# Optimization experiments

Measured on AMD Instinct MI355X. Metric: run time of the kernel, lower is better.

## Reference

```python
import jax, jax.numpy as jnp
import numpy as np

K = 6
N_LEVELS = [200000, 50000, 12500]
CHANNELS = [3, 64, 128, 256]
DEGREE = 32
FANIN = 4          # each pooled node averages FANIN fine nodes (D values = 1/FANIN)
NUM_CLASSES = 10


def setup_inputs() -> dict:
    key = jax.random.key(0)
    ks = jax.random.split(key, 16)
    inp = {}
    inp["x"] = jax.random.normal(ks[0], (N_LEVELS[0], 3), dtype=jnp.float32)
    # random sparse connectivity per level (edge lists, COO)
    for i, n in enumerate(N_LEVELS):
        inp[f"edge_index{i}"] = jax.random.randint(ks[1 + i], (2, n * DEGREE), 0, n)
    # sparse downscale matrices: row r of D_i averages FANIN source nodes
    inp["pool_cols0"] = jax.random.randint(ks[4], (N_LEVELS[1] * FANIN,), 0, N_LEVELS[0])
    inp["pool_cols1"] = jax.random.randint(ks[5], (N_LEVELS[2] * FANIN,), 0, N_LEVELS[1])
    # ChebConv parameters: weight [K, in, out] (Glorot-ish), bias [out]
    for i in range(3):
        cin, cout = CHANNELS[i], CHANNELS[i + 1]
        scale = (2.0 / (cin + cout)) ** 0.5
        inp[f"w{i}"] = scale * jax.random.normal(ks[6 + 2 * i], (K, cin, cout), dtype=jnp.float32)
        inp[f"b{i}"] = jnp.zeros((cout,), dtype=jnp.float32)
    lin_in = N_LEVELS[-1] * CHANNELS[-1]
    inp["lw"] = jax.random.normal(ks[12], (NUM_CLASSES, lin_in), dtype=jnp.float32) * (1.0 / np.sqrt(lin_in))
    inp["lb"] = jnp.zeros((NUM_CLASSES,), dtype=jnp.float32)
    return inp


def cheb_conv(x, edge_index, weight, bias):
    """PyG ChebConv, sym normalization, lambda_max=2, unit edge weights.
    Scaled Laplacian reduces to L_hat = -D^{-1/2} A D^{-1/2} (zero diagonal)."""
    row, col = edge_index[0], edge_index[1]
    n = x.shape[0]
    w = (row != col).astype(x.dtype)                 # remove_self_loops
    deg = jax.ops.segment_sum(w, row, num_segments=n)
    dinv = jnp.where(deg > 0, jax.lax.rsqrt(deg), 0.0)
    norm = -w * dinv[row] * dinv[col]                # [E]

    def prop(h):  # scatter-add of norm * gathered source features
        return jax.ops.segment_sum(norm[:, None] * h[col], row, num_segments=n)

    Tx0 = x
    out = Tx0 @ weight[0]
    Tx1 = prop(x)
    out = out + Tx1 @ weight[1]
    for k in range(2, weight.shape[0]):
        Tx2 = 2.0 * prop(Tx1) - Tx0
        out = out + Tx2 @ weight[k]
        Tx0, Tx1 = Tx1, Tx2
    return out + bias


def pool(x, cols, n_out):
    # sparse.mm(D, x) with D having FANIN entries of 1/FANIN per row (rows sorted)
    return x[cols].reshape(n_out, FANIN, x.shape[1]).mean(axis=1)


def reference(x, edge_index0, edge_index1, edge_index2, pool_cols0, pool_cols1,
              w0, b0, w1, b1, w2, b2, lw, lb):
    h = jax.nn.relu(cheb_conv(x, edge_index0, w0, b0))
    h = pool(h, pool_cols0, N_LEVELS[1])
    h = jax.nn.relu(cheb_conv(h, edge_index1, w1, b1))
    h = pool(h, pool_cols1, N_LEVELS[2])
    h = cheb_conv(h, edge_index2, w2, b2)
    return lw @ h.reshape(-1) + lb   # F.linear on flattened features -> [num_classes]
```

## Files before the change

kernel.cpp:

```cpp
#include <hip/hip_runtime.h>
#include <hip/hip_bf16.h>


#define N0 200000
#define N1 50000
#define N2 12500
#define KCH 6
#define NCLS 10

#define SB 8
#define BROWS 256
#define BCAP 10240
#define NBUK_MAX 800
#define NBLK 1024
#define TILE_MAX 6250

typedef __hip_bfloat16 bf16;
typedef _Float16 f16;
typedef f16 f16x2 __attribute__((ext_vector_type(2)));
typedef f16 f16x4 __attribute__((ext_vector_type(4)));
typedef f16 f16x8 __attribute__((ext_vector_type(8)));
typedef float f32x4 __attribute__((ext_vector_type(4)));

static __device__ __forceinline__ float b2f(bf16 v) { return __bfloat162float(v); }
static __device__ __forceinline__ float blo(unsigned u) { return __uint_as_float(u << 16); }
static __device__ __forceinline__ float bhi(unsigned u) { return __uint_as_float(u & 0xFFFF0000u); }

struct BLvl {
    const int* rows; const int* cols;
    int* cntBB; int* btot; int* bbase;
    unsigned* colB; int* colS; int* ptr; float* dinv;
    int E, nbuk, tile, n;
};

__global__ void detect_k(const unsigned int* __restrict__ xb, int* __restrict__ flag) {
    __shared__ int cs;
    int t = threadIdx.x;
    if (t == 0) cs = 0;
    __syncthreads();
    unsigned w = xb[t];
    unsigned e = (w >> 7) & 0xFFu;
    if (e >= 0x30u && e <= 0x43u) atomicAdd(&cs, 1);
    __syncthreads();
    if (t == 0) flag[0] = (cs < 128) ? 1 : 0;
}

__global__ __launch_bounds__(256) void convw2_k(const void* __restrict__ W1, f16* __restrict__ wT1,
                                                const void* __restrict__ W2, f16* __restrict__ wT2,
                                                const int* __restrict__ flag) {
    int isf = flag[0];
    int idx = blockIdx.x * 256 + threadIdx.x;
    const int tot1 = 384 * 128;
    const int tot2 = 768 * 256;
    if (idx < tot1) {
        int n2 = idx / 384, k = idx - n2 * 384;
        float v;
        if (isf) v = ((const float*)W1)[(size_t)k * 128 + n2];
        else     v = b2f(((const bf16*)W1)[(size_t)k * 128 + n2]);
        wT1[idx] = (f16)v;
    } else if (idx < tot1 + tot2) {
        int i2 = idx - tot1;
        int n2 = i2 / 768, k = i2 - n2 * 768;
        float v;
        if (isf) v = ((const float*)W2)[(size_t)k * 256 + n2];
        else     v = b2f(((const bf16*)W2)[(size_t)k * 256 + n2]);
        wT2[i2] = (f16)v;
    }
}


__global__ __launch_bounds__(256) void binH3_k(BLvl a, BLvl b, BLvl c) {
    BLvl lv = (blockIdx.y == 0) ? a : ((blockIdx.y == 1) ? b : c);
    __shared__ int cnt[NBUK_MAX];
    int t = threadIdx.x;
    for (int i = t; i < lv.nbuk; i += 256) cnt[i] = 0;
    __syncthreads();
    int beg = blockIdx.x * lv.tile;
    int end = beg + lv.tile;
    if (end > lv.E) end = lv.E;
    for (int idx = beg + t; idx < end; idx += 256) {
        int r = lv.rows[idx], cc = lv.cols[idx];
        if (r != cc) atomicAdd(&cnt[r >> SB], 1);
    }
    __syncthreads();
    for (int i = t; i < lv.nbuk; i += 256) lv.cntBB[(size_t)blockIdx.x * lv.nbuk + i] = cnt[i];
}

__global__ __launch_bounds__(256) void scanBB3_k(BLvl a, BLvl b, BLvl c) {
    __shared__ int ps[256];
    int gb = blockIdx.x, t = threadIdx.x;
    BLvl lv; int b0;
    if (gb < a.nbuk) { lv = a; b0 = gb; }
    else if (gb < a.nbuk + b.nbuk) { lv = b; b0 = gb - a.nbuk; }
    else { lv = c; b0 = gb - a.nbuk - b.nbuk; }
    int vals[4];
    int pt = 0;
#pragma unroll
    for (int i = 0; i < 4; ++i) { vals[i] = lv.cntBB[(size_t)(4 * t + i) * lv.nbuk + b0]; pt += vals[i]; }
    ps[t] = pt;
    __syncthreads();
    for (int off = 1; off < 256; off <<= 1) {
        int x = (t >= off) ? ps[t - off] : 0;
        __syncthreads();
        ps[t] += x;
        __syncthreads();
    }
    int ex = ps[t] - pt;
#pragma unroll
    for (int i = 0; i < 4; ++i) { lv.cntBB[(size_t)(4 * t + i) * lv.nbuk + b0] = ex; ex += vals[i]; }
    if (t == 255) lv.btot[b0] = ps[255];
}

__global__ __launch_bounds__(1024) void scanb3_k(BLvl a, BLvl b, BLvl c, float* __restrict__ accum) {
    __shared__ int s[1024];
    BLvl lv = (blockIdx.x == 0) ? a : ((blockIdx.x == 1) ? b : c);
    int t = threadIdx.x;
    if (blockIdx.x == 0 && t < 16) accum[t] = 0.f;
    int v = (t < lv.nbuk) ? lv.btot[t] : 0;
    s[t] = v;
    __syncthreads();
    for (int off = 1; off < 1024; off <<= 1) {
        int x = (t >= off) ? s[t - off] : 0;
        __syncthreads();
        s[t] += x;
        __syncthreads();
    }
    if (t < lv.nbuk) lv.bbase[t] = s[t] - v;
    if (t == 1023) lv.ptr[lv.n] = s[1023];
}

__global__ __launch_bounds__(256) void binS3_k(BLvl a, BLvl b, BLvl c) {
    BLvl lv = (blockIdx.y == 0) ? a : ((blockIdx.y == 1) ? b : c);
    __shared__ int lcnt[NBUK_MAX];
    __shared__ int lexc[NBUK_MAX];
    __shared__ int lfill[NBUK_MAX];
    __shared__ int gstart[NBUK_MAX];
    __shared__ int ps[256];
    __shared__ unsigned scol[TILE_MAX];
    int t = threadIdx.x;
    for (int i = t; i < lv.nbuk; i += 256) { lcnt[i] = 0; lfill[i] = 0; }
    __syncthreads();
    int beg = blockIdx.x * lv.tile;
    int end = beg + lv.tile;
    if (end > lv.E) end = lv.E;
    for (int idx = beg + t; idx < end; idx += 256) {
        int r = lv.rows[idx], cc = lv.cols[idx];
        if (r != cc) atomicAdd(&lcnt[r >> SB], 1);
    }
    __syncthreads();
    int idx4 = 4 * t;
    int c4[4];
#pragma unroll
    for (int i = 0; i < 4; ++i) c4[i] = (idx4 + i < lv.nbuk) ? lcnt[idx4 + i] : 0;
    int tot = c4[0] + c4[1] + c4[2] + c4[3];
    ps[t] = tot;
    __syncthreads();
    for (int off = 1; off < 256; off <<= 1) {
        int x = (t >= off) ? ps[t - off] : 0;
        __syncthreads();
        ps[t] += x;
        __syncthreads();
    }
    int run = ps[t] - tot;
#pragma unroll
    for (int i = 0; i < 4; ++i) {
        if (idx4 + i < lv.nbuk) lexc[idx4 + i] = run;
        run += c4[i];
    }
    for (int i = t; i < lv.nbuk; i += 256) gstart[i] = lv.bbase[i] + lv.cntBB[(size_t)blockIdx.x * lv.nbuk + i];
    __syncthreads();
    for (int idx = beg + t; idx < end; idx += 256) {
        int r = lv.rows[idx], cc = lv.cols[idx];
        if (r != cc) {
            int bk = r >> SB;
            int s = atomicAdd(&lfill[bk], 1);
            scol[lexc[bk] + s] = ((unsigned)(r & (BROWS - 1)) << 18) | (unsigned)cc;
        }
    }
    __syncthreads();
    int wv = t >> 6, lane = t & 63;
    for (int bk = wv; bk < lv.nbuk; bk += 4) {
        int cnt2 = lcnt[bk];
        int lsrc = lexc[bk], gdst = gstart[bk];
        for (int i = lane; i < cnt2; i += 64) lv.colB[gdst + i] = scol[lsrc + i];
    }
}

__global__ __launch_bounds__(256) void binB3_k(BLvl a, BLvl b, BLvl c,
                                               const void* __restrict__ x, f16* __restrict__ TxAll,
                                               f16x4* __restrict__ G0, const int* __restrict__ flag) {
    __shared__ int lcnt[BROWS];
    __shared__ int lexc[BROWS];
    __shared__ int lfill[BROWS];
    __shared__ int scol[BCAP];
    int gb = blockIdx.x;
    int t = threadIdx.x;
    BLvl lv; int b0, lvl;
    if (gb < a.nbuk) { lv = a; b0 = gb; lvl = 0; }
    else if (gb < a.nbuk + b.nbuk) { lv = b; b0 = gb - a.nbuk; lvl = 1; }
    else { lv = c; b0 = gb - a.nbuk - b.nbuk; lvl = 2; }
    int rowbase = b0 << SB;
    int rowend = rowbase + BROWS;
    if (rowend > lv.n) rowend = lv.n;
    int nrows = rowend - rowbase;
    int count = lv.btot[b0];
    int base = lv.bbase[b0];
    const unsigned* slab = lv.colB + base;
    lcnt[t] = 0;
    __syncthreads();
    for (int i = t; i < count; i += 256) atomicAdd(&lcnt[slab[i] >> 18], 1);
    __syncthreads();
    int v = lcnt[t];
    lexc[t] = v;
    __syncthreads();
    for (int off = 1; off < 256; off <<= 1) {
        int xx = (t >= off) ? lexc[t - off] : 0;
        __syncthreads();
        lexc[t] += xx;
        __syncthreads();
    }
    int excl = lexc[t] - v;
    __syncthreads();
    lexc[t] = excl;
    __syncthreads();
    if (t < nrows) {
        lv.ptr[rowbase + t] = base + excl;
        float dr = (v > 0) ? rsqrtf((float)v) : 0.f;
        lv.dinv[rowbase + t] = dr;
        if (lvl == 0) {
            int r = rowbase + t;
            int isf = flag[0];
            float v0, v1, v2;
            if (isf) {
                const float* xf = (const float*)x;
                v0 = xf[3 * r]; v1 = xf[3 * r + 1]; v2 = xf[3 * r + 2];
            } else {
                const bf16* xh = (const bf16*)x;
                v0 = b2f(xh[3 * r]); v1 = b2f(xh[3 * r + 1]); v2 = b2f(xh[3 * r + 2]);
            }
            f16x4 pk = {(f16)v0, (f16)v1, (f16)v2, (f16)dr};
            *(f16x4*)(TxAll + (size_t)r * 24) = pk;
            G0[r] = pk;
        }
    }
    int nh = (count <= BCAP) ? 1 : 2;
    int rspan = BROWS / nh;
    for (int h = 0; h < nh; ++h) {
        int rowLo = h * rspan, rowHi = rowLo + rspan;
        int segOff = lexc[rowLo];
        int segEnd = (rowHi >= BROWS) ? count : lexc[rowHi];
        int segCnt = segEnd - segOff;
        lfill[t] = 0;
        __syncthreads();
        for (int i = t; i < count; i += 256) {
            unsigned pk = slab[i];
            int rl = pk >> 18;
            if (rl >= rowLo && rl < rowHi) {
                int s = atomicAdd(&lfill[rl], 1);
                scol[lexc[rl] + s - segOff] = (int)(pk & 0x3FFFFu);
            }
        }
        __syncthreads();
        for (int i = t; i < segCnt; i += 256) lv.colS[base + segOff + i] = scol[i];
        __syncthreads();
    }
}


__global__ __launch_bounds__(256) void prop_narrow_k(const int* __restrict__ ptr, const int* __restrict__ colS,
                                                     const float* __restrict__ dinv,
                                                     const f16x4* __restrict__ gin, f16x4* __restrict__ gout,
                                                     f16* __restrict__ oslot,
                                                     int n, float alpha, int useSub) {
    int wv = threadIdx.x >> 6, half = (threadIdx.x >> 5) & 1, sl = threadIdx.x & 31;
    int r = blockIdx.x * 8 + wv * 2 + half;
    if (r >= n) return;
    int s = ptr[r], e = ptr[r + 1];
    float dr = dinv[r];
    float a0 = 0.f, a1 = 0.f, a2 = 0.f;
    for (int idx = s + sl; idx < e; idx += 32) {
        int c = colS[idx];
        f16x4 h = gin[c];
        float nrm = -dr * (float)h.w;
        a0 += nrm * (float)h.x;
        a1 += nrm * (float)h.y;
        a2 += nrm * (float)h.z;
    }
#pragma unroll
    for (int off2 = 16; off2 > 0; off2 >>= 1) {
        a0 += __shfl_xor(a0, off2);
        a1 += __shfl_xor(a1, off2);
        a2 += __shfl_xor(a2, off2);
    }
    if (sl == 0) {
        float v0 = alpha * a0, v1 = alpha * a1, v2 = alpha * a2;
        if (useSub) {
            f16x4 sv = gout[r];
            v0 -= (float)sv.x; v1 -= (float)sv.y; v2 -= (float)sv.z;
        }
        f16x4 ov = {(f16)v0, (f16)v1, (f16)v2, (f16)dr};
        gout[r] = ov;
        *(f16x4*)(oslot + (size_t)r * 24) = ov;
    }
}

__global__ __launch_bounds__(256) void prop_wide2_k(const int* __restrict__ ptr, const int* __restrict__ colS,
                                                    const float* __restrict__ dinv, const f16* __restrict__ hin,
                                                    const f16* __restrict__ sub, f16* __restrict__ o,
                                                    int ld, int n, float alpha, int useSub) {
    int wv = threadIdx.x >> 6, lane = threadIdx.x & 63;
    int p = lane >> 5, q = lane & 31;
    int r = blockIdx.x * 4 + wv;
    if (r >= n) return;
    int s = ptr[r], e = ptr[r + 1];
    float dr = dinv[r];
    float ax = 0.f, ay = 0.f;
    for (int base = s; base < e; base += 64) {
        int idx = base + lane;
        int c = 0;
        float dc = 0.f;
        if (idx < e) { c = colS[idx]; dc = dinv[c]; }
        int cnt2 = e - base;
        if (cnt2 > 64) cnt2 = 64;
        int j = 0;
        for (; j + 4 <= cnt2; j += 4) {
            int j0 = j + p, j1 = j + 2 + p;
            int c0 = __shfl(c, j0), c1 = __shfl(c, j1);
            float n0 = -dr * __shfl(dc, j0), n1 = -dr * __shfl(dc, j1);
            f16x2 h0 = *(const f16x2*)(hin + (size_t)c0 * ld + 2 * q);
            f16x2 h1 = *(const f16x2*)(hin + (size_t)c1 * ld + 2 * q);
            ax += n0 * (float)h0.x + n1 * (float)h1.x;
            ay += n0 * (float)h0.y + n1 * (float)h1.y;
        }
        for (; j < cnt2; j += 2) {
            int jj = j + p;
            int valid = jj < cnt2;
            int cc = __shfl(c, valid ? jj : 0);
            float nd = __shfl(dc, valid ? jj : 0);
            float nrm = valid ? -dr * nd : 0.f;
            f16x2 h = *(const f16x2*)(hin + (size_t)cc * ld + 2 * q);
            ax += nrm * (float)h.x;
            ay += nrm * (float)h.y;
        }
    }
    ax += __shfl_xor(ax, 32);
    ay += __shfl_xor(ay, 32);
    if (p == 0) {
        size_t rb = (size_t)r * ld + 2 * q;
        float vx = alpha * ax, vy = alpha * ay;
        if (useSub) {
            f16x2 sv = *(const f16x2*)(sub + rb);
            vx -= (float)sv.x; vy -= (float)sv.y;
        }
        f16x2 ov = {(f16)vx, (f16)vy};
        *(f16x2*)(o + rb) = ov;
    }
}

__global__ __launch_bounds__(256) void prop_wide1h_k(const int* __restrict__ ptr, const int* __restrict__ colS,
                                                     const float* __restrict__ dinv, const f16* __restrict__ hin,
                                                     const f16* __restrict__ sub, f16* __restrict__ o,
                                                     int ld, int n, float alpha, int useSub) {
    int wv = threadIdx.x >> 6, lane = threadIdx.x & 63;
    int r = blockIdx.x * 4 + wv;
    if (r >= n) return;
    int s = ptr[r], e = ptr[r + 1];
    float dr = dinv[r];
    float ax = 0.f, ay = 0.f;
    for (int base = s; base < e; base += 64) {
        int idx = base + lane;
        int c = 0;
        float dc = 0.f;
        if (idx < e) { c = colS[idx]; dc = dinv[c]; }
        int cnt2 = e - base;
        if (cnt2 > 64) cnt2 = 64;
        int j = 0;
        for (; j + 4 <= cnt2; j += 4) {
            int c0 = __shfl(c, j), c1 = __shfl(c, j + 1), c2 = __shfl(c, j + 2), c3 = __shfl(c, j + 3);
            float n0 = -dr * __shfl(dc, j), n1 = -dr * __shfl(dc, j + 1);
            float n2 = -dr * __shfl(dc, j + 2), n3 = -dr * __shfl(dc, j + 3);
            f16x2 h0 = *(const f16x2*)(hin + (size_t)c0 * ld + 2 * lane);
            f16x2 h1 = *(const f16x2*)(hin + (size_t)c1 * ld + 2 * lane);
            f16x2 h2 = *(const f16x2*)(hin + (size_t)c2 * ld + 2 * lane);
            f16x2 h3 = *(const f16x2*)(hin + (size_t)c3 * ld + 2 * lane);
            ax += n0 * (float)h0.x + n1 * (float)h1.x + n2 * (float)h2.x + n3 * (float)h3.x;
            ay += n0 * (float)h0.y + n1 * (float)h1.y + n2 * (float)h2.y + n3 * (float)h3.y;
        }
        for (; j < cnt2; ++j) {
            int cc = __shfl(c, j);
            float nrm = -dr * __shfl(dc, j);
            f16x2 h = *(const f16x2*)(hin + (size_t)cc * ld + 2 * lane);
            ax += nrm * (float)h.x;
            ay += nrm * (float)h.y;
        }
    }
    size_t rb = (size_t)r * ld + 2 * lane;
    float vx = alpha * ax, vy = alpha * ay;
    if (useSub) {
        f16x2 sv = *(const f16x2*)(sub + rb);
        vx -= (float)sv.x; vy -= (float)sv.y;
    }
    f16x2 ov = {(f16)vx, (f16)vy};
    *(f16x2*)(o + rb) = ov;
}


__global__ __launch_bounds__(256) void gemm_mfma2_k(const f16* __restrict__ A, int lda,
                                                    const f16* __restrict__ WT,
                                                    const void* __restrict__ bias,
                                                    void* __restrict__ C, int M, int N, int K, int flags,
                                                    const int* __restrict__ flag) {
    __shared__ f16 As[64][40];
    __shared__ f16 Bs[64][40];
    int isf = flag[0];
    int t = threadIdx.x;
    int w = t >> 6, l = t & 63, q = l >> 4, m16 = l & 15;
    int m0 = blockIdx.y * 64, n0 = blockIdx.x * 64;
    f32x4 acc[4] = {};
    for (int k0 = 0; k0 < K; k0 += 32) {
        {
            int row = t >> 2, cg = (t & 3) * 8;
            int gm = m0 + row;
            f16x8 av = {};
            if (gm < M) av = *(const f16x8*)(A + (size_t)gm * lda + k0 + cg);
            *(f16x8*)&As[row][cg] = av;
        }
        {
            int nr = t >> 2, cg = (t & 3) * 8;
            f16x8 bv = *(const f16x8*)(WT + (size_t)(n0 + nr) * K + k0 + cg);
            *(f16x8*)&Bs[nr][cg] = bv;
        }
        __syncthreads();
        f16x8 aa = *(const f16x8*)&As[w * 16 + m16][q * 8];
        f16x8 b0 = *(const f16x8*)&Bs[m16][q * 8];
        f16x8 b1 = *(const f16x8*)&Bs[16 + m16][q * 8];
        f16x8 b2 = *(const f16x8*)&Bs[32 + m16][q * 8];
        f16x8 b3 = *(const f16x8*)&Bs[48 + m16][q * 8];
        acc[0] = __builtin_amdgcn_mfma_f32_16x16x32_f16(aa, b0, acc[0], 0, 0, 0);
        acc[1] = __builtin_amdgcn_mfma_f32_16x16x32_f16(aa, b1, acc[1], 0, 0, 0);
        acc[2] = __builtin_amdgcn_mfma_f32_16x16x32_f16(aa, b2, acc[2], 0, 0, 0);
        acc[3] = __builtin_amdgcn_mfma_f32_16x16x32_f16(aa, b3, acc[3], 0, 0, 0);
        __syncthreads();
    }
#pragma unroll
    for (int tile = 0; tile < 4; ++tile) {
        int gn = n0 + tile * 16 + m16;
        float bv = 0.f;
        if (flags & 4) {
            if (isf) bv = ((const float*)bias)[gn];
            else     bv = b2f(((const bf16*)bias)[gn]);
        }
#pragma unroll
        for (int i = 0; i < 4; ++i) {
            int gm = m0 + w * 16 + q * 4 + i;
            if (gm < M) {
                float v = acc[tile][i] + bv;
                if (flags & 1) v = fmaxf(v, 0.f);
                size_t ci = (size_t)gm * N + gn;
                if (flags & 16) ((f16*)C)[ci] = (f16)v;
                else            ((float*)C)[ci] = v;
            }
        }
    }
}


__global__ __launch_bounds__(256) void gemm_k(const f16* __restrict__ A, int lda,
                                              const void* __restrict__ W,
                                              const void* __restrict__ bias,
                                              void* __restrict__ C, int M, int N, int K, int flags,
                                              const int* __restrict__ flag) {
    __shared__ float As[16][65];
    __shared__ float Ws[16][64];
    int isf = flag[0];
    int pack3 = flags & 8;
    int t = threadIdx.x;
    int tn = t & 15, tm = t >> 4;
    int m0 = blockIdx.y * 64, n0 = blockIdx.x * 64;
    float acc[4][4] = {};
    for (int k0 = 0; k0 < K; k0 += 16) {
#pragma unroll
        for (int i = 0; i < 4; ++i) {
            int idx = i * 256 + t;
            int m = idx >> 4, k = idx & 15;
            int gm = m0 + m, gk = k0 + k;
            int phys = pack3 ? (gk + gk / 3) : gk;
            As[k][m] = (gm < M && gk < K) ? (float)A[(size_t)gm * lda + phys] : 0.f;
        }
        if (isf) {
            const float* Wf = (const float*)W;
#pragma unroll
            for (int i = 0; i < 4; ++i) {
                int idx = i * 256 + t;
                int k = idx >> 6, nn = idx & 63;
                int gk = k0 + k;
                Ws[k][nn] = (gk < K) ? Wf[(size_t)gk * N + n0 + nn] : 0.f;
            }
        } else {
            const bf16* Wh = (const bf16*)W;
#pragma unroll
            for (int i = 0; i < 4; ++i) {
                int idx = i * 256 + t;
                int k = idx >> 6, nn = idx & 63;
                int gk = k0 + k;
                Ws[k][nn] = (gk < K) ? b2f(Wh[(size_t)gk * N + n0 + nn]) : 0.f;
            }
        }
        __syncthreads();
#pragma unroll
        for (int kk = 0; kk < 16; ++kk) {
            float aa[4], bb[4];
#pragma unroll
            for (int i = 0; i < 4; ++i) aa[i] = As[kk][tm * 4 + i];
#pragma unroll
            for (int j = 0; j < 4; ++j) bb[j] = Ws[kk][tn * 4 + j];
#pragma unroll
            for (int i = 0; i < 4; ++i)
#pragma unroll
                for (int j = 0; j < 4; ++j) acc[i][j] += aa[i] * bb[j];
        }
        __syncthreads();
    }
#pragma unroll
    for (int i = 0; i < 4; ++i) {
        int gm = m0 + tm * 4 + i;
        if (gm >= M) continue;
#pragma unroll
        for (int j = 0; j < 4; ++j) {
            int gn = n0 + tn * 4 + j;
            size_t ci = (size_t)gm * N + gn;
            float v = acc[i][j];
            if (flags & 4) {
                if (isf) v += ((const float*)bias)[gn];
                else     v += b2f(((const bf16*)bias)[gn]);
            }
            if (flags & 1) v = fmaxf(v, 0.f);
            if (flags & 16) ((f16*)C)[ci] = (f16)v;
            else            ((float*)C)[ci] = v;
        }
    }
}


__global__ __launch_bounds__(256) void pool_k(const f16* __restrict__ in, const int* __restrict__ pcols,
                                              f16* __restrict__ out, int n_out, int C, int ld) {
    int idx = blockIdx.x * 256 + threadIdx.x;
    int C4 = C >> 2;
    if (idx >= n_out * C4) return;
    int r = idx / C4, c4 = (idx - r * C4) * 4;
    const int* pc = pcols + (size_t)r * 4;
    float s0 = 0.f, s1 = 0.f, s2 = 0.f, s3 = 0.f;
#pragma unroll
    for (int f = 0; f < 4; ++f) {
        f16x4 v = *(const f16x4*)(in + (size_t)pc[f] * C + c4);
        s0 += (float)v.x; s1 += (float)v.y; s2 += (float)v.z; s3 += (float)v.w;
    }
    f16x4 o = {(f16)(0.25f * s0), (f16)(0.25f * s1), (f16)(0.25f * s2), (f16)(0.25f * s3)};
    *(f16x4*)(out + (size_t)r * ld + c4) = o;
}


__global__ __launch_bounds__(256) void linear10b_k(const float* __restrict__ h, const void* __restrict__ lw,
                                                   float* __restrict__ accum, int LIN, const int* __restrict__ flag) {
    int isf = flag[0];
    int t = threadIdx.x;
    int nvec = LIN >> 3;
    int stride = gridDim.x * 256;
    float p[NCLS];
#pragma unroll
    for (int c = 0; c < NCLS; ++c) p[c] = 0.f;
    const float4* h4 = (const float4*)h;
    if (isf) {
        const float4* lw4 = (const float4*)lw;
        size_t ro = (size_t)(LIN >> 2);
        for (int i = blockIdx.x * 256 + t; i < nvec; i += stride) {
            float4 a0 = h4[2 * i], a1 = h4[2 * i + 1];
#pragma unroll
            for (int c = 0; c < NCLS; ++c) {
                float4 b0v = lw4[c * ro + 2 * i], b1v = lw4[c * ro + 2 * i + 1];
                p[c] += a0.x * b0v.x + a0.y * b0v.y + a0.z * b0v.z + a0.w * b0v.w
                      + a1.x * b1v.x + a1.y * b1v.y + a1.z * b1v.z + a1.w * b1v.w;
            }
        }
    } else {
        const uint4* lwv = (const uint4*)lw;
        size_t ro = (size_t)nvec;
        for (int i = blockIdx.x * 256 + t; i < nvec; i += stride) {
            float4 a0 = h4[2 * i], a1 = h4[2 * i + 1];
#pragma unroll
            for (int c = 0; c < NCLS; ++c) {
                uint4 w4 = lwv[c * ro + i];
                p[c] += a0.x * blo(w4.x) + a0.y * bhi(w4.x)
                      + a0.z * blo(w4.y) + a0.w * bhi(w4.y)
                      + a1.x * blo(w4.z) + a1.y * bhi(w4.z)
                      + a1.z * blo(w4.w) + a1.w * bhi(w4.w);
            }
        }
    }
    __shared__ float wsum[4][NCLS];
    int wv = t >> 6, lane = t & 63;
#pragma unroll
    for (int c = 0; c < NCLS; ++c) {
        float v = p[c];
        for (int off2 = 32; off2 > 0; off2 >>= 1) v += __shfl_down(v, off2);
        if (lane == 0) wsum[wv][c] = v;
    }
    __syncthreads();
    if (t < NCLS) {
        float s = wsum[0][t] + wsum[1][t] + wsum[2][t] + wsum[3][t];
        unsafeAtomicAdd(&accum[t], s);
    }
}

__global__ void finalize_k(const float* __restrict__ accum, const void* __restrict__ lb,
                           void* __restrict__ outp, const int* __restrict__ flag) {
    int isf = flag[0];
    int t = threadIdx.x;
    if (t < NCLS) {
        float lbv;
        if (isf) lbv = ((const float*)lb)[t];
        else     lbv = b2f(((const bf16*)lb)[t]);
        float v = accum[t] + lbv;
        if (isf) ((float*)outp)[t] = v;
        else     ((bf16*)outp)[t] = __float2bfloat16(v);
    }
}

__global__ void diag_k(void* __restrict__ outp, float val, const int* __restrict__ flag) {
    int isf = flag[0];
    int t = threadIdx.x;
    if (t < NCLS) {
        if (isf) ((float*)outp)[t] = val;
        else     ((bf16*)outp)[t] = __float2bfloat16(val);
    }
}


extern "C" void kernel_launch(void* const* d_in, const int* in_sizes, int n_in,
                              void* d_out, int out_size, void* d_ws, size_t ws_size,
                              hipStream_t stream) {
    const void* x  = d_in[0];
    const int* ei0 = (const int*)d_in[1];
    const int* ei1 = (const int*)d_in[2];
    const int* ei2 = (const int*)d_in[3];
    const int* pc0 = (const int*)d_in[4];
    const int* pc1 = (const int*)d_in[5];
    const void* w0 = d_in[6];
    const void* b0 = d_in[7];
    const void* w1 = d_in[8];
    const void* b1 = d_in[9];
    const void* w2 = d_in[10];
    const void* b2 = d_in[11];
    const void* lw = d_in[12];
    const void* lb = d_in[13];

    const int E0 = in_sizes[1] / 2, E1 = in_sizes[2] / 2, E2 = in_sizes[3] / 2;
    const int Ns[3] = {N0, N1, N2};
    const int Es[3] = {E0, E1, E2};

    char* base = (char*)d_ws;
    size_t off = 0;
    auto alloc = [&](size_t bytes) -> void* {
        void* p = base + off;
        off += (bytes + 255) & ~(size_t)255;
        return p;
    };
    f16*      TxAll = (f16*)alloc((size_t)19200000 * 2);
    float*    OutB  = (float*)alloc((size_t)12800000 * 4);
    f16*      OutBh = (f16*)OutB;
    f16x4*    G0    = (f16x4*)alloc((size_t)N0 * 8);
    f16x4*    G1    = (f16x4*)alloc((size_t)N0 * 8);
    f16*      wT1   = (f16*)alloc((size_t)384 * 128 * 2);
    f16*      wT2   = (f16*)alloc((size_t)768 * 256 * 2);
    float*    accum = (float*)alloc(64);
    int*      flag  = (int*)(accum + 16);

    BLvl BL[3];
    for (int i = 0; i < 3; ++i) {
        int n = Ns[i], E = Es[i];
        BL[i].nbuk = (n + BROWS - 1) >> SB;
        BL[i].tile = (E + NBLK - 1) / NBLK;
        BL[i].E = E;
        BL[i].n = n;
        BL[i].cntBB = (int*)alloc((size_t)NBLK * BL[i].nbuk * 4);
        BL[i].btot  = (int*)alloc((size_t)BL[i].nbuk * 4);
        BL[i].bbase = (int*)alloc((size_t)BL[i].nbuk * 4);
        BL[i].colB  = (unsigned*)alloc((size_t)E * 4);
        BL[i].colS  = (int*)alloc((size_t)E * 4);
        BL[i].ptr   = (int*)alloc((size_t)(n + 1) * 4);
        BL[i].dinv  = (float*)alloc((size_t)n * 4);
    }
    BL[0].rows = ei0; BL[0].cols = ei0 + E0;
    BL[1].rows = ei1; BL[1].cols = ei1 + E1;
    BL[2].rows = ei2; BL[2].cols = ei2 + E2;

    detect_k<<<1, 256, 0, stream>>>((const unsigned int*)x, flag);

    if (ws_size < off) {
        diag_k<<<1, 64, 0, stream>>>(d_out, (float)(ws_size >> 20), flag);
        return;
    }

    convw2_k<<<(384 * 128 + 768 * 256 + 255) / 256, 256, 0, stream>>>(w1, wT1, w2, wT2, flag);

    int nbukT = BL[0].nbuk + BL[1].nbuk + BL[2].nbuk;
    binH3_k<<<dim3(NBLK, 3), 256, 0, stream>>>(BL[0], BL[1], BL[2]);
    scanBB3_k<<<nbukT, 256, 0, stream>>>(BL[0], BL[1], BL[2]);
    scanb3_k<<<3, 1024, 0, stream>>>(BL[0], BL[1], BL[2], accum);
    binS3_k<<<dim3(NBLK, 3), 256, 0, stream>>>(BL[0], BL[1], BL[2]);
    binB3_k<<<nbukT, 256, 0, stream>>>(BL[0], BL[1], BL[2], x, TxAll, G0, flag);

    struct Lvl {
        int n, cin, cout;
        const void *w, *b;
        int relu;
    };
    Lvl L[3] = {
        {N0, 3, 64, w0, b0, 1},
        {N1, 64, 128, w1, b1, 1},
        {N2, 128, 256, w2, b2, 0},
    };
    f16x4* G[2] = {G0, G1};

    for (int li = 0; li < 3; ++li) {
        const Lvl& v = L[li];
        int n = v.n, cin = v.cin, cout = v.cout;
        int ld = (li == 0) ? 24 : KCH * cin;
        int slot = (li == 0) ? 4 : cin;
        const int* ptr = BL[li].ptr;
        const int* colS = BL[li].colS;
        const float* dinv = BL[li].dinv;

        for (int k = 1; k < KCH; ++k) {
            float alpha = (k >= 2) ? 2.f : 1.f;
            if (li == 0) {
                prop_narrow_k<<<(n + 7) / 8, 256, 0, stream>>>(ptr, colS, dinv,
                                                               G[(k - 1) & 1], G[k & 1],
                                                               TxAll + (size_t)k * 4, n, alpha, k >= 2);
            } else {
                const f16* hin = TxAll + (size_t)(k - 1) * slot;
                const f16* sub = (k >= 2) ? (TxAll + (size_t)(k - 2) * slot) : nullptr;
                f16* o = TxAll + (size_t)k * slot;
                if (cin == 64)
                    prop_wide2_k<<<(n + 3) / 4, 256, 0, stream>>>(ptr, colS, dinv, hin, sub, o, ld, n, alpha, k >= 2);
                else
                    prop_wide1h_k<<<(n + 3) / 4, 256, 0, stream>>>(ptr, colS, dinv, hin, sub, o, ld, n, alpha, k >= 2);
            }
        }

        dim3 gg(cout / 64, (n + 63) / 64);
        int f16out = (li < 2) ? 16 : 0;
        if (li == 0)
            gemm_k<<<gg, 256, 0, stream>>>(TxAll, ld, v.w, v.b, OutB, n, cout, KCH * cin,
                                           4 | 8 | f16out | (v.relu ? 1 : 0), flag);
        else
            gemm_mfma2_k<<<gg, 256, 0, stream>>>(TxAll, ld, (li == 1) ? wT1 : wT2, v.b, OutB, n, cout, KCH * cin,
                                                 4 | f16out | (v.relu ? 1 : 0), flag);

        if (li == 0)
            pool_k<<<(N1 * 16 + 255) / 256, 256, 0, stream>>>(OutBh, pc0, TxAll, N1, 64, KCH * 64);
        else if (li == 1)
            pool_k<<<(N2 * 32 + 255) / 256, 256, 0, stream>>>(OutBh, pc1, TxAll, N2, 128, KCH * 128);
    }

    {
        dim3 lg(512);
        linear10b_k<<<lg, 256, 0, stream>>>(OutB, lw, accum, N2 * 256, flag);
    }
    finalize_k<<<1, 64, 0, stream>>>(accum, lb, d_out, flag);
}
```

Measured before the change: 971.4 us.

## Replace two-pass deterministic edge binning with single-pass atomic scatter into fixed-capacity slabs

The histogram, per-bucket scan and local-sort scatter kernels that bucket edges by row block are replaced with one grid-stride kernel. It reserves slots with global atomics on padded per-bucket counters and writes packed entries into fixed-capacity slabs. This removes one full read pass over the edge lists and two kernel launches, at the cost of heavily contended global atomics and a memset. Slab capacity is a hard cap (BCAPS), so a bucket whose count exceeds it would silently drop edges, and entry order within a bucket is no longer deterministic.

```diff
diff --git a/kernel.cpp b/kernel.cpp
--- a/kernel.cpp
+++ b/kernel.cpp
@@ -11,9 +11,8 @@
 #define SB 8
 #define BROWS 256
 #define BCAP 10240
+#define BCAPS 12800
 #define NBUK_MAX 800
-#define NBLK 1024
-#define TILE_MAX 6250
 
 typedef __hip_bfloat16 bf16;
 typedef _Float16 f16;
@@ -28,9 +27,8 @@
 
 struct BLvl {
     const int* rows; const int* cols;
-    int* cntBB; int* btot; int* bbase;
-    unsigned* colB; int* colS; int* ptr; float* dinv;
-    int E, nbuk, tile, n;
+    int* bbase; int* colS; int* ptr; float* dinv;
+    int E, nbuk, n;
 };
 
 __global__ void detect_k(const unsigned int* __restrict__ xb, int* __restrict__ flag) {
@@ -69,54 +67,35 @@
 }
 
 
-__global__ __launch_bounds__(256) void binH3_k(BLvl a, BLvl b, BLvl c) {
-    BLvl lv = (blockIdx.y == 0) ? a : ((blockIdx.y == 1) ? b : c);
-    __shared__ int cnt[NBUK_MAX];
-    int t = threadIdx.x;
-    for (int i = t; i < lv.nbuk; i += 256) cnt[i] = 0;
-    __syncthreads();
-    int beg = blockIdx.x * lv.tile;
-    int end = beg + lv.tile;
-    if (end > lv.E) end = lv.E;
-    for (int idx = beg + t; idx < end; idx += 256) {
-        int r = lv.rows[idx], cc = lv.cols[idx];
-        if (r != cc) atomicAdd(&cnt[r >> SB], 1);
-    }
-    __syncthreads();
-    for (int i = t; i < lv.nbuk; i += 256) lv.cntBB[(size_t)blockIdx.x * lv.nbuk + i] = cnt[i];
-}
-
-__global__ __launch_bounds__(256) void scanBB3_k(BLvl a, BLvl b, BLvl c) {
-    __shared__ int ps[256];
-    int gb = blockIdx.x, t = threadIdx.x;
-    BLvl lv; int b0;
-    if (gb < a.nbuk) { lv = a; b0 = gb; }
-    else if (gb < a.nbuk + b.nbuk) { lv = b; b0 = gb - a.nbuk; }
-    else { lv = c; b0 = gb - a.nbuk - b.nbuk; }
-    int vals[4];
-    int pt = 0;
-#pragma unroll
-    for (int i = 0; i < 4; ++i) { vals[i] = lv.cntBB[(size_t)(4 * t + i) * lv.nbuk + b0]; pt += vals[i]; }
-    ps[t] = pt;
-    __syncthreads();
-    for (int off = 1; off < 256; off <<= 1) {
-        int x = (t >= off) ? ps[t - off] : 0;
-        __syncthreads();
-        ps[t] += x;
-        __syncthreads();
-    }
-    int ex = ps[t] - pt;
-#pragma unroll
-    for (int i = 0; i < 4; ++i) { lv.cntBB[(size_t)(4 * t + i) * lv.nbuk + b0] = ex; ex += vals[i]; }
-    if (t == 255) lv.btot[b0] = ps[255];
-}
-
-__global__ __launch_bounds__(1024) void scanb3_k(BLvl a, BLvl b, BLvl c, float* __restrict__ accum) {
+__global__ __launch_bounds__(256) void scat3_k(BLvl a, BLvl b, BLvl c,
+                                               int* __restrict__ bcnt, unsigned* __restrict__ colBg) {
+    int tid = blockIdx.x * 256 + threadIdx.x;
+    int stride = gridDim.x * 256;
+    int lvlbase = 0;
+    for (int l = 0; l < 3; ++l) {
+        const BLvl& lv = (l == 0) ? a : ((l == 1) ? b : c);
+        for (int idx = tid; idx < lv.E; idx += stride) {
+            int r = lv.rows[idx], cc = lv.cols[idx];
+            if (r != cc) {
+                int gb = lvlbase + (r >> SB);
+                int s = atomicAdd(&bcnt[gb * 16], 1);
+                if (s < BCAPS)
+                    colBg[(size_t)gb * BCAPS + s] = ((unsigned)(r & (BROWS - 1)) << 18) | (unsigned)cc;
+            }
+        }
+        lvlbase += lv.nbuk;
+    }
+}
+
+__global__ __launch_bounds__(1024) void scanb3_k(BLvl a, BLvl b, BLvl c,
+                                                 const int* __restrict__ bcnt, float* __restrict__ accum) {
     __shared__ int s[1024];
-    BLvl lv = (blockIdx.x == 0) ? a : ((blockIdx.x == 1) ? b : c);
-    int t = threadIdx.x;
-    if (blockIdx.x == 0 && t < 16) accum[t] = 0.f;
-    int v = (t < lv.nbuk) ? lv.btot[t] : 0;
+    int lvl = blockIdx.x;
+    BLvl lv = (lvl == 0) ? a : ((lvl == 1) ? b : c);
+    int lvlbase = (lvl == 0) ? 0 : ((lvl == 1) ? a.nbuk : a.nbuk + b.nbuk);
+    int t = threadIdx.x;
+    if (lvl == 0 && t < 16) accum[t] = 0.f;
+    int v = (t < lv.nbuk) ? bcnt[(lvlbase + t) * 16] : 0;
     s[t] = v;
     __syncthreads();
     for (int off = 1; off < 1024; off <<= 1) {
@@ -129,64 +108,8 @@
     if (t == 1023) lv.ptr[lv.n] = s[1023];
 }
 
-__global__ __launch_bounds__(256) void binS3_k(BLvl a, BLvl b, BLvl c) {
-    BLvl lv = (blockIdx.y == 0) ? a : ((blockIdx.y == 1) ? b : c);
-    __shared__ int lcnt[NBUK_MAX];
-    __shared__ int lexc[NBUK_MAX];
-    __shared__ int lfill[NBUK_MAX];
-    __shared__ int gstart[NBUK_MAX];
-    __shared__ int ps[256];
-    __shared__ unsigned scol[TILE_MAX];
-    int t = threadIdx.x;
-    for (int i = t; i < lv.nbuk; i += 256) { lcnt[i] = 0; lfill[i] = 0; }
-    __syncthreads();
-    int beg = blockIdx.x * lv.tile;
-    int end = beg + lv.tile;
-    if (end > lv.E) end = lv.E;
-    for (int idx = beg + t; idx < end; idx += 256) {
-        int r = lv.rows[idx], cc = lv.cols[idx];
-        if (r != cc) atomicAdd(&lcnt[r >> SB], 1);
-    }
-    __syncthreads();
-    int idx4 = 4 * t;
-    int c4[4];
-#pragma unroll
-    for (int i = 0; i < 4; ++i) c4[i] = (idx4 + i < lv.nbuk) ? lcnt[idx4 + i] : 0;
-    int tot = c4[0] + c4[1] + c4[2] + c4[3];
-    ps[t] = tot;
-    __syncthreads();
-    for (int off = 1; off < 256; off <<= 1) {
-        int x = (t >= off) ? ps[t - off] : 0;
-        __syncthreads();
-        ps[t] += x;
-        __syncthreads();
-    }
-    int run = ps[t] - tot;
-#pragma unroll
-    for (int i = 0; i < 4; ++i) {
-        if (idx4 + i < lv.nbuk) lexc[idx4 + i] = run;
-        run += c4[i];
-    }
-    for (int i = t; i < lv.nbuk; i += 256) gstart[i] = lv.bbase[i] + lv.cntBB[(size_t)blockIdx.x * lv.nbuk + i];
-    __syncthreads();
-    for (int idx = beg + t; idx < end; idx += 256) {
-        int r = lv.rows[idx], cc = lv.cols[idx];
-        if (r != cc) {
-            int bk = r >> SB;
-            int s = atomicAdd(&lfill[bk], 1);
-            scol[lexc[bk] + s] = ((unsigned)(r & (BROWS - 1)) << 18) | (unsigned)cc;
-        }
-    }
-    __syncthreads();
-    int wv = t >> 6, lane = t & 63;
-    for (int bk = wv; bk < lv.nbuk; bk += 4) {
-        int cnt2 = lcnt[bk];
-        int lsrc = lexc[bk], gdst = gstart[bk];
-        for (int i = lane; i < cnt2; i += 64) lv.colB[gdst + i] = scol[lsrc + i];
-    }
-}
-
 __global__ __launch_bounds__(256) void binB3_k(BLvl a, BLvl b, BLvl c,
+                                               const int* __restrict__ bcnt, const unsigned* __restrict__ colBg,
                                                const void* __restrict__ x, f16* __restrict__ TxAll,
                                                f16x4* __restrict__ G0, const int* __restrict__ flag) {
     __shared__ int lcnt[BROWS];
@@ -203,9 +126,10 @@
     int rowend = rowbase + BROWS;
     if (rowend > lv.n) rowend = lv.n;
     int nrows = rowend - rowbase;
-    int count = lv.btot[b0];
+    int count = bcnt[gb * 16];
+    if (count > BCAPS) count = BCAPS;
     int base = lv.bbase[b0];
-    const unsigned* slab = lv.colB + base;
+    const unsigned* slab = colBg + (size_t)gb * BCAPS;
     lcnt[t] = 0;
     __syncthreads();
     for (int i = t; i < count; i += 256) atomicAdd(&lcnt[slab[i] >> 18], 1);
@@ -676,24 +600,25 @@
     int*      flag  = (int*)(accum + 16);
 
     BLvl BL[3];
+    int nbukT = 0;
     for (int i = 0; i < 3; ++i) {
         int n = Ns[i], E = Es[i];
         BL[i].nbuk = (n + BROWS - 1) >> SB;
-        BL[i].tile = (E + NBLK - 1) / NBLK;
         BL[i].E = E;
         BL[i].n = n;
-        BL[i].cntBB = (int*)alloc((size_t)NBLK * BL[i].nbuk * 4);
-        BL[i].btot  = (int*)alloc((size_t)BL[i].nbuk * 4);
         BL[i].bbase = (int*)alloc((size_t)BL[i].nbuk * 4);
-        BL[i].colB  = (unsigned*)alloc((size_t)E * 4);
         BL[i].colS  = (int*)alloc((size_t)E * 4);
         BL[i].ptr   = (int*)alloc((size_t)(n + 1) * 4);
         BL[i].dinv  = (float*)alloc((size_t)n * 4);
+        nbukT += BL[i].nbuk;
     }
     BL[0].rows = ei0; BL[0].cols = ei0 + E0;
     BL[1].rows = ei1; BL[1].cols = ei1 + E1;
     BL[2].rows = ei2; BL[2].cols = ei2 + E2;
 
+    int*      bcnt  = (int*)alloc((size_t)nbukT * 64);
+    unsigned* colBg = (unsigned*)alloc((size_t)nbukT * BCAPS * 4);
+
     detect_k<<<1, 256, 0, stream>>>((const unsigned int*)x, flag);
 
     if (ws_size < off) {
@@ -703,12 +628,10 @@
 
     convw2_k<<<(384 * 128 + 768 * 256 + 255) / 256, 256, 0, stream>>>(w1, wT1, w2, wT2, flag);
 
-    int nbukT = BL[0].nbuk + BL[1].nbuk + BL[2].nbuk;
-    binH3_k<<<dim3(NBLK, 3), 256, 0, stream>>>(BL[0], BL[1], BL[2]);
-    scanBB3_k<<<nbukT, 256, 0, stream>>>(BL[0], BL[1], BL[2]);
-    scanb3_k<<<3, 1024, 0, stream>>>(BL[0], BL[1], BL[2], accum);
-    binS3_k<<<dim3(NBLK, 3), 256, 0, stream>>>(BL[0], BL[1], BL[2]);
-    binB3_k<<<nbukT, 256, 0, stream>>>(BL[0], BL[1], BL[2], x, TxAll, G0, flag);
+    hipMemsetAsync(bcnt, 0, (size_t)nbukT * 64, stream);
+    scat3_k<<<2048, 256, 0, stream>>>(BL[0], BL[1], BL[2], bcnt, colBg);
+    scanb3_k<<<3, 1024, 0, stream>>>(BL[0], BL[1], BL[2], bcnt, accum);
+    binB3_k<<<nbukT, 256, 0, stream>>>(BL[0], BL[1], BL[2], bcnt, colBg, x, TxAll, G0, flag);
 
     struct Lvl {
         int n, cin, cout;
```

After: 1.333 ms. 37.2% more time.
